# Performance work log

Measured on AMD Instinct MI355X. Metric: run time of the kernel, lower is better.

The kernel has to match this reference:

```python
import jax, jax.numpy as jnp
import numpy as np

B, N, D, DN, F, NUM_F, O, H = 8, 4096, 256, 128, 128, 1024, 8, 1024
EPS = 1e-5

def setup_inputs() -> dict:
    key = jax.random.key(0)
    ks = jax.random.split(key, 10)
    s = 0.02
    x = jax.random.normal(ks[0], (B, N, D), dtype=jnp.float32)
    ctx = jax.random.normal(ks[1], (B, DN), dtype=jnp.float32)
    idx = jax.random.randint(ks[2], (F,), 0, NUM_F, dtype=jnp.int64)
    cond_w = jax.random.normal(ks[3], (DN, 2 * D), dtype=jnp.float32) * s
    cond_b = jnp.zeros((2 * D,), dtype=jnp.float32)
    ffn_w_in = jax.random.normal(ks[4], (D, 2 * H), dtype=jnp.float32) * s
    ffn_b_in = jnp.zeros((2 * H,), dtype=jnp.float32)
    ffn_w_out = jax.random.normal(ks[5], (H, D), dtype=jnp.float32) * s
    ffn_b_out = jnp.zeros((D,), dtype=jnp.float32)
    emb = jax.random.normal(ks[6], (NUM_F, D * O), dtype=jnp.float32) * s
    return {"x": x, "ctx": ctx, "idx": idx, "cond_w": cond_w, "cond_b": cond_b,
            "ffn_w_in": ffn_w_in, "ffn_b_in": ffn_b_in,
            "ffn_w_out": ffn_w_out, "ffn_b_out": ffn_b_out, "emb": emb}

def reference(x, ctx, idx, cond_w, cond_b, ffn_w_in, ffn_b_in, ffn_w_out, ffn_b_out, emb):
    # Conditional LayerNorm: normalize over last dim, FiLM-style modulation from ctx
    mu = jnp.mean(x, axis=-1, keepdims=True)
    var = jnp.mean((x - mu) ** 2, axis=-1, keepdims=True)
    h = (x - mu) * jax.lax.rsqrt(var + EPS)                      # [B,N,D]
    ss = ctx @ cond_w + cond_b                                   # [B,2D]
    scale, shift = jnp.split(ss, 2, axis=-1)                     # [B,D] each
    h = h * (1.0 + scale[:, None, :]) + shift[:, None, :]
    # Gated FFN: in-proj -> (gelu(gate) * value) -> out-proj
    uv = h @ ffn_w_in + ffn_b_in                                 # [B,N,2H]
    u, v = jnp.split(uv, 2, axis=-1)
    y = (jax.nn.gelu(u) * v) @ ffn_w_out + ffn_b_out             # [B,N,D]
    # Embedding-generated per-feature output weights, then batched contraction
    w = emb[idx].reshape(F, D, O)                                # gather [F,D,O]
    out = jnp.einsum('bnd,fdo->bnfo', y, w)                      # [B,N,F,O]
    return out
```

## Files before the change

### kernel.cpp

```cpp
#include <hip/hip_runtime.h>
#include <cstdint>
#include <cstddef>

#define M_TOT 32768
#define D_    256
#define DN_   128
#define TWO_D 512
#define H_    1024
#define TWO_H 2048

typedef unsigned short ushort_t;
typedef __attribute__((ext_vector_type(8))) short bf16x8;
typedef __attribute__((ext_vector_type(4))) float f32x4;

__device__ __forceinline__ ushort_t f2bf(float f) {
  union { float f; uint32_t i; } v; v.f = f;
  uint32_t r = v.i + 0x7fffu + ((v.i >> 16) & 1u);
  return (ushort_t)(r >> 16);
}

__device__ __forceinline__ void async_ld16(const void* g, void* l) {
  __builtin_amdgcn_global_load_lds(
      (const __attribute__((address_space(1))) void*)g,
      (__attribute__((address_space(3))) void*)l, 16, 0, 0);
}

__global__ __launch_bounds__(256) void cond_ss_kernel(
    const float* __restrict__ ctx, const float* __restrict__ cond_w,
    const float* __restrict__ cond_b, float* __restrict__ ss) {
  int j = blockIdx.x * 256 + threadIdx.x;
  int b = j >> 9, col = j & 511;
  float acc = cond_b[col];
  for (int k = 0; k < DN_; ++k)
    acc += ctx[b * DN_ + k] * cond_w[k * TWO_D + col];
  ss[j] = acc;
}

__global__ __launch_bounds__(256) void transpose_f32_bf16_kernel(
    const float* __restrict__ in, ushort_t* __restrict__ out, int R, int C) {
  __shared__ float T[64 * 65];
  int ctiles = C >> 6;
  int bi = blockIdx.x / ctiles, bj = blockIdx.x % ctiles;
  int r0 = bi * 64, c0 = bj * 64;
  int tid = threadIdx.x;
#pragma unroll
  for (int it = 0; it < 16; ++it) {
    int idx = it * 256 + tid;
    int r = idx >> 6, c = idx & 63;
    T[r * 65 + c] = in[(size_t)(r0 + r) * C + c0 + c];
  }
  __syncthreads();
#pragma unroll
  for (int it = 0; it < 8; ++it) {
    int idx = it * 256 + tid;
    int a = idx >> 5;
    int b = (idx & 31) * 2;
    uint32_t pk = (uint32_t)f2bf(T[b * 65 + a]) |
                  ((uint32_t)f2bf(T[(b + 1) * 65 + a]) << 16);
    *(uint32_t*)&out[(size_t)(c0 + a) * R + r0 + b] = pk;
  }
}

__global__ __launch_bounds__(256) void gather_emb_kernel(
    const float* __restrict__ emb, const int* __restrict__ idx,
    ushort_t* __restrict__ W2T) {
  int f = blockIdx.x;
  bool looks64 = (idx[1] == 0) & (idx[3] == 0) & (idx[5] == 0) & (idx[7] == 0);
  int fi = looks64 ? idx[2 * f] : idx[f];
  const float* src = emb + (size_t)fi * 2048;
  int o = threadIdx.x >> 5, d0 = (threadIdx.x & 31) * 8;
  ushort_t buf[8];
#pragma unroll
  for (int k = 0; k < 8; ++k) buf[k] = f2bf(src[(d0 + k) * 8 + o]);
  *(bf16x8*)&W2T[(size_t)(f * 8 + o) * 256 + d0] = *(bf16x8*)buf;
}

__global__ __launch_bounds__(256) void ln_film_kernel(
    const float* __restrict__ x, const float* __restrict__ ss,
    ushort_t* __restrict__ h) {
  int row = blockIdx.x * 4 + (threadIdx.x >> 6);
  int lane = threadIdx.x & 63;
  int b = row >> 12;
  const float* xr = x + (size_t)row * D_;
  float4 pk = *(const float4*)(xr + lane * 4);
  float f0 = pk.x, f1 = pk.y, f2 = pk.z, f3 = pk.w;
  float s = f0 + f1 + f2 + f3;
  float q = f0 * f0 + f1 * f1 + f2 * f2 + f3 * f3;
#pragma unroll
  for (int off = 32; off > 0; off >>= 1) {
    s += __shfl_xor(s, off, 64);
    q += __shfl_xor(q, off, 64);
  }
  float mean = s * (1.0f / 256.0f);
  float var = q * (1.0f / 256.0f) - mean * mean;
  float rs = rsqrtf(var + 1e-5f);
  int d = lane * 4;
  const float* ssb = ss + b * TWO_D;
  float o0 = (f0 - mean) * rs * (1.0f + ssb[d + 0]) + ssb[256 + d + 0];
  float o1 = (f1 - mean) * rs * (1.0f + ssb[d + 1]) + ssb[256 + d + 1];
  float o2 = (f2 - mean) * rs * (1.0f + ssb[d + 2]) + ssb[256 + d + 2];
  float o3 = (f3 - mean) * rs * (1.0f + ssb[d + 3]) + ssb[256 + d + 3];
  uint2 st;
  st.x = (uint32_t)f2bf(o0) | ((uint32_t)f2bf(o1) << 16);
  st.y = (uint32_t)f2bf(o2) | ((uint32_t)f2bf(o3) << 16);
  *(uint2*)(h + (size_t)row * D_ + lane * 4) = st;
}

template <bool BIAS, bool OUT_F32>
__global__ __launch_bounds__(256, 2) void gemm_bt_kernel(
    const ushort_t* __restrict__ A, const ushort_t* __restrict__ BT,
    const float* __restrict__ bias, void* __restrict__ Cout,
    int M, int N, int K) {
  __shared__ ushort_t As[128 * 32];
  __shared__ ushort_t Bs[128 * 32];
  __shared__ float Cs[64 * 132];
  const int tid = threadIdx.x, lane = tid & 63, wave = tid >> 6;
  const int wm = wave >> 1, wn = wave & 1;
  const int m0 = blockIdx.x * 128, n0 = blockIdx.y * 128;
  const int srow = lane >> 2, sch = (lane & 3) * 8;
  f32x4 acc[4][4] = {};
  for (int k0 = 0; k0 < K; k0 += 32) {
    for (int i = wave; i < 8; i += 4) {
      async_ld16(A + (size_t)(m0 + i * 16 + srow) * K + k0 + sch, &As[i * 512]);
      async_ld16(BT + (size_t)(n0 + i * 16 + srow) * K + k0 + sch, &Bs[i * 512]);
    }
    __syncthreads();
    bf16x8 a[4], b[4];
#pragma unroll
    for (int i = 0; i < 4; ++i)
      a[i] = *(const bf16x8*)&As[(wm * 64 + i * 16 + (lane & 15)) * 32 + (lane >> 4) * 8];
#pragma unroll
    for (int j = 0; j < 4; ++j)
      b[j] = *(const bf16x8*)&Bs[(wn * 64 + j * 16 + (lane & 15)) * 32 + (lane >> 4) * 8];
#pragma unroll
    for (int i = 0; i < 4; ++i)
#pragma unroll
      for (int j = 0; j < 4; ++j)
        acc[i][j] = __builtin_amdgcn_mfma_f32_16x16x32_bf16(a[i], b[j], acc[i][j], 0, 0, 0);
    __syncthreads();
  }
#pragma unroll
  for (int p = 0; p < 2; ++p) {
    __syncthreads();
    if (wm == p) {
#pragma unroll
      for (int j = 0; j < 4; ++j) {
        int col = wn * 64 + j * 16 + (lane & 15);
        float bv = BIAS ? bias[n0 + col] : 0.0f;
#pragma unroll
        for (int i = 0; i < 4; ++i) {
          int rl = i * 16 + ((lane >> 4) << 2);
#pragma unroll
          for (int r = 0; r < 4; ++r)
            Cs[(rl + r) * 132 + col] = acc[i][j][r] + bv;
        }
      }
    }
    __syncthreads();
#pragma unroll
    for (int it = 0; it < 8; ++it) {
      int t = it * 256 + tid;
      int r = t >> 5, c = (t & 31) * 4;
      float4 v = *(const float4*)&Cs[r * 132 + c];
      size_t off = (size_t)(m0 + p * 64 + r) * N + n0 + c;
      if (OUT_F32) {
        *(float4*)((float*)Cout + off) = v;
      } else {
        ushort4 s4;
        s4.x = f2bf(v.x); s4.y = f2bf(v.y); s4.z = f2bf(v.z); s4.w = f2bf(v.w);
        *(ushort4*)((ushort_t*)Cout + off) = s4;
      }
    }
  }
}

__global__ __launch_bounds__(256, 2) void gemm_gated_kernel(
    const ushort_t* __restrict__ A,
    const ushort_t* __restrict__ WinT,
    const float* __restrict__ bin,
    ushort_t* __restrict__ G) {
  __shared__ ushort_t As[128 * 32];
  __shared__ ushort_t Bus[64 * 32];
  __shared__ ushort_t Bvs[64 * 32];
  __shared__ float Cs[64 * 68];
  const int tid = threadIdx.x, lane = tid & 63, wave = tid >> 6;
  const int wm = wave >> 1, wn = wave & 1;
  const int m0 = blockIdx.x * 128;
  const int j0 = blockIdx.y * 64;
  const int srow = lane >> 2, sch = (lane & 3) * 8;
  const int K = 256;
  f32x4 au[4][2] = {}, av[4][2] = {};
  for (int k0 = 0; k0 < K; k0 += 32) {
    for (int i = wave; i < 8; i += 4)
      async_ld16(A + (size_t)(m0 + i * 16 + srow) * K + k0 + sch, &As[i * 512]);
    {
      int i = wave;
      async_ld16(WinT + (size_t)(j0 + i * 16 + srow) * K + k0 + sch, &Bus[i * 512]);
      async_ld16(WinT + (size_t)(1024 + j0 + i * 16 + srow) * K + k0 + sch, &Bvs[i * 512]);
    }
    __syncthreads();
    bf16x8 a[4], bu[2], bv[2];
#pragma unroll
    for (int i = 0; i < 4; ++i)
      a[i] = *(const bf16x8*)&As[(wm * 64 + i * 16 + (lane & 15)) * 32 + (lane >> 4) * 8];
#pragma unroll
    for (int j = 0; j < 2; ++j) {
      bu[j] = *(const bf16x8*)&Bus[(wn * 32 + j * 16 + (lane & 15)) * 32 + (lane >> 4) * 8];
      bv[j] = *(const bf16x8*)&Bvs[(wn * 32 + j * 16 + (lane & 15)) * 32 + (lane >> 4) * 8];
    }
#pragma unroll
    for (int i = 0; i < 4; ++i)
#pragma unroll
      for (int j = 0; j < 2; ++j) {
        au[i][j] = __builtin_amdgcn_mfma_f32_16x16x32_bf16(a[i], bu[j], au[i][j], 0, 0, 0);
        av[i][j] = __builtin_amdgcn_mfma_f32_16x16x32_bf16(a[i], bv[j], av[i][j], 0, 0, 0);
      }
    __syncthreads();
  }
#pragma unroll
  for (int p = 0; p < 2; ++p) {
    __syncthreads();
    if (wm == p) {
#pragma unroll
      for (int j = 0; j < 2; ++j) {
        int col = wn * 32 + j * 16 + (lane & 15);
        float bub = bin[j0 + col];
        float bvb = bin[1024 + j0 + col];
#pragma unroll
        for (int i = 0; i < 4; ++i) {
          int rl = i * 16 + ((lane >> 4) << 2);
#pragma unroll
          for (int r = 0; r < 4; ++r) {
            float u = au[i][j][r] + bub;
            float v = av[i][j][r] + bvb;
            float t = 0.7978845608028654f * (u + 0.044715f * u * u * u);
            float e = __expf(2.0f * t);
            float th = 1.0f - 2.0f / (e + 1.0f);
            float gl = 0.5f * u * (1.0f + th);
            Cs[(rl + r) * 68 + col] = gl * v;
          }
        }
      }
    }
    __syncthreads();
#pragma unroll
    for (int it = 0; it < 4; ++it) {
      int t = it * 256 + tid;
      int r = t >> 4, c = (t & 15) * 4;
      float4 v = *(const float4*)&Cs[r * 68 + c];
      ushort4 s4;
      s4.x = f2bf(v.x); s4.y = f2bf(v.y); s4.z = f2bf(v.z); s4.w = f2bf(v.w);
      *(ushort4*)&G[(size_t)(m0 + p * 64 + r) * 1024 + j0 + c] = s4;
    }
  }
}

extern "C" void kernel_launch(void* const* d_in, const int* in_sizes, int n_in,
                              void* d_out, int out_size, void* d_ws, size_t ws_size,
                              hipStream_t stream) {
  const float* x      = (const float*)d_in[0];
  const float* ctx    = (const float*)d_in[1];
  const int*   idx    = (const int*)d_in[2];
  const float* cond_w = (const float*)d_in[3];
  const float* cond_b = (const float*)d_in[4];
  const float* w_in   = (const float*)d_in[5];
  const float* b_in   = (const float*)d_in[6];
  const float* w_out  = (const float*)d_in[7];
  const float* b_out  = (const float*)d_in[8];
  const float* emb    = (const float*)d_in[9];

  char* w = (char*)d_ws;
  float* ss = (float*)w;           w += (size_t)8 * TWO_D * 4;
  ushort_t* h = (ushort_t*)w;      w += (size_t)M_TOT * D_ * 2;
  ushort_t* y = (ushort_t*)w;      w += (size_t)M_TOT * D_ * 2;
  ushort_t* WinT = (ushort_t*)w;   w += (size_t)TWO_H * D_ * 2;
  ushort_t* WoutT = (ushort_t*)w;  w += (size_t)D_ * H_ * 2;
  ushort_t* W2T = (ushort_t*)w;    w += (size_t)H_ * D_ * 2;
  ushort_t* g = (ushort_t*)d_out;

  cond_ss_kernel<<<16, 256, 0, stream>>>(ctx, cond_w, cond_b, ss);
  transpose_f32_bf16_kernel<<<(D_ / 64) * (TWO_H / 64), 256, 0, stream>>>(w_in, WinT, D_, TWO_H);
  transpose_f32_bf16_kernel<<<(H_ / 64) * (D_ / 64), 256, 0, stream>>>(w_out, WoutT, H_, D_);
  gather_emb_kernel<<<128, 256, 0, stream>>>(emb, idx, W2T);
  ln_film_kernel<<<M_TOT / 4, 256, 0, stream>>>(x, ss, h);
  gemm_gated_kernel<<<dim3(256, 16), 256, 0, stream>>>(h, WinT, b_in, g);
  gemm_bt_kernel<true, false><<<dim3(256, 2), 256, 0, stream>>>(g, WoutT, b_out, y, M_TOT, 256, 1024);
  gemm_bt_kernel<false, true><<<dim3(256, 8), 256, 0, stream>>>(y, W2T, nullptr, d_out, M_TOT, 1024, 256);
}
```

Before: 319.3 us.

## Fuse gated FFN in-proj and out-proj into one kernel keeping intermediate on-chip

Replaces the separate gated in-projection GEMM and the out-projection GEMM with one fused kernel. Each 64-row block keeps its LN output in LDS and loops over H in chunks of 64, computing the gelu-gated intermediate into LDS and accumulating the 256-wide output in registers. This removes the write and re-read of the 32768x1024 bf16 intermediate through global memory. The final GEMM now loads K in steps of 64 to halve barrier count. In exchange the fused kernel uses smaller M tiles, many barriers per block, large LDS footprint (lower occupancy), and only 512 blocks, which may hurt MFMA utilization.

```diff
diff --git a/kernel.cpp b/kernel.cpp
--- a/kernel.cpp
+++ b/kernel.cpp
@@ -106,37 +106,140 @@
   *(uint2*)(h + (size_t)row * D_ + lane * 4) = st;
 }
 
-template <bool BIAS, bool OUT_F32>
-__global__ __launch_bounds__(256, 2) void gemm_bt_kernel(
+__global__ __launch_bounds__(256, 2) void ffn_fused_kernel(
+    const ushort_t* __restrict__ h,
+    const ushort_t* __restrict__ WinT,
+    const float* __restrict__ bin,
+    const ushort_t* __restrict__ WoutT,
+    const float* __restrict__ bout,
+    ushort_t* __restrict__ y) {
+  __shared__ ushort_t Ah[64 * 256];
+  __shared__ ushort_t Sh[64 * 264];
+  __shared__ ushort_t Gs[64 * 72];
+  const int tid = threadIdx.x, lane = tid & 63, wave = tid >> 6;
+  const int r = lane >> 2, q = lane & 3;
+  const int l15 = lane & 15, l4 = lane >> 4;
+  const int m0 = blockIdx.x * 64;
+  const int fragoff = l15 * 32 + l4 * 8;
+
+  for (int t = wave; t < 32; t += 4) {
+    int rt = t & 3, kc = t >> 2;
+    async_ld16(h + (size_t)(m0 + rt * 16 + r) * 256 + kc * 32 + q * 8, &Ah[t * 512]);
+  }
+
+  f32x4 yac[16] = {};
+
+  for (int j = 0; j < 16; ++j) {
+    f32x4 uac[4] = {}, vac[4] = {};
+#pragma unroll
+    for (int s = 0; s < 2; ++s) {
+      __syncthreads();
+      for (int t = wave; t < 16; t += 4) {
+        int rt = t & 3, kc = t >> 2;
+        size_t grow = (size_t)(j * 64 + rt * 16 + r);
+        async_ld16(WinT + grow * 256 + s * 128 + kc * 32 + q * 8, &Sh[t * 512]);
+        async_ld16(WinT + (grow + 1024) * 256 + s * 128 + kc * 32 + q * 8, &Sh[(16 + t) * 512]);
+      }
+      __syncthreads();
+#pragma unroll
+      for (int ks = 0; ks < 4; ++ks) {
+        bf16x8 af = *(const bf16x8*)&Ah[((s * 4 + ks) * 4 + wave) * 512 + fragoff];
+#pragma unroll
+        for (int jt = 0; jt < 4; ++jt) {
+          bf16x8 bu = *(const bf16x8*)&Sh[(ks * 4 + jt) * 512 + fragoff];
+          bf16x8 bv = *(const bf16x8*)&Sh[(16 + ks * 4 + jt) * 512 + fragoff];
+          uac[jt] = __builtin_amdgcn_mfma_f32_16x16x32_bf16(af, bu, uac[jt], 0, 0, 0);
+          vac[jt] = __builtin_amdgcn_mfma_f32_16x16x32_bf16(af, bv, vac[jt], 0, 0, 0);
+        }
+      }
+    }
+#pragma unroll
+    for (int jt = 0; jt < 4; ++jt) {
+      int col = jt * 16 + l15;
+      float bub = bin[j * 64 + col];
+      float bvb = bin[1024 + j * 64 + col];
+#pragma unroll
+      for (int rr = 0; rr < 4; ++rr) {
+        float u = uac[jt][rr] + bub;
+        float v = vac[jt][rr] + bvb;
+        float t = 0.7978845608028654f * (u + 0.044715f * u * u * u);
+        float e = __expf(2.0f * t);
+        float th = 1.0f - 2.0f / (e + 1.0f);
+        float gl = 0.5f * u * (1.0f + th);
+        Gs[(wave * 16 + l4 * 4 + rr) * 72 + col] = f2bf(gl * v);
+      }
+    }
+    __syncthreads();
+    for (int t = wave; t < 32; t += 4) {
+      int nt = t & 15, s2 = t >> 4;
+      async_ld16(WoutT + (size_t)(nt * 16 + r) * 1024 + j * 64 + s2 * 32 + q * 8, &Sh[t * 512]);
+    }
+    __syncthreads();
+#pragma unroll
+    for (int s2 = 0; s2 < 2; ++s2) {
+      bf16x8 gf = *(const bf16x8*)&Gs[(wave * 16 + l15) * 72 + s2 * 32 + l4 * 8];
+#pragma unroll
+      for (int nt = 0; nt < 16; ++nt) {
+        bf16x8 bw = *(const bf16x8*)&Sh[(s2 * 16 + nt) * 512 + fragoff];
+        yac[nt] = __builtin_amdgcn_mfma_f32_16x16x32_bf16(gf, bw, yac[nt], 0, 0, 0);
+      }
+    }
+  }
+  __syncthreads();
+#pragma unroll
+  for (int nt = 0; nt < 16; ++nt) {
+    int col = nt * 16 + l15;
+    float bb = bout[col];
+#pragma unroll
+    for (int rr = 0; rr < 4; ++rr)
+      Sh[(wave * 16 + l4 * 4 + rr) * 264 + col] = f2bf(yac[nt][rr] + bb);
+  }
+  __syncthreads();
+#pragma unroll
+  for (int it = 0; it < 8; ++it) {
+    int id = it * 256 + tid;
+    int rr = id >> 5, cc = id & 31;
+    bf16x8 vv = *(const bf16x8*)&Sh[rr * 264 + cc * 8];
+    *(bf16x8*)&y[(size_t)(m0 + rr) * 256 + cc * 8] = vv;
+  }
+}
+
+__global__ __launch_bounds__(256, 2) void gemm_out_kernel(
     const ushort_t* __restrict__ A, const ushort_t* __restrict__ BT,
-    const float* __restrict__ bias, void* __restrict__ Cout,
-    int M, int N, int K) {
-  __shared__ ushort_t As[128 * 32];
-  __shared__ ushort_t Bs[128 * 32];
+    float* __restrict__ C) {
+  __shared__ ushort_t As[128 * 64];
+  __shared__ ushort_t Bs[128 * 64];
   __shared__ float Cs[64 * 132];
   const int tid = threadIdx.x, lane = tid & 63, wave = tid >> 6;
   const int wm = wave >> 1, wn = wave & 1;
   const int m0 = blockIdx.x * 128, n0 = blockIdx.y * 128;
-  const int srow = lane >> 2, sch = (lane & 3) * 8;
+  const int r = lane >> 2, q = lane & 3;
+  const int l15 = lane & 15, l4 = lane >> 4;
+  const int fragoff = l15 * 32 + l4 * 8;
+  const int N = 1024, K = 256;
   f32x4 acc[4][4] = {};
-  for (int k0 = 0; k0 < K; k0 += 32) {
-    for (int i = wave; i < 8; i += 4) {
-      async_ld16(A + (size_t)(m0 + i * 16 + srow) * K + k0 + sch, &As[i * 512]);
-      async_ld16(BT + (size_t)(n0 + i * 16 + srow) * K + k0 + sch, &Bs[i * 512]);
-    }
-    __syncthreads();
-    bf16x8 a[4], b[4];
-#pragma unroll
-    for (int i = 0; i < 4; ++i)
-      a[i] = *(const bf16x8*)&As[(wm * 64 + i * 16 + (lane & 15)) * 32 + (lane >> 4) * 8];
-#pragma unroll
-    for (int j = 0; j < 4; ++j)
-      b[j] = *(const bf16x8*)&Bs[(wn * 64 + j * 16 + (lane & 15)) * 32 + (lane >> 4) * 8];
-#pragma unroll
-    for (int i = 0; i < 4; ++i)
-#pragma unroll
-      for (int j = 0; j < 4; ++j)
-        acc[i][j] = __builtin_amdgcn_mfma_f32_16x16x32_bf16(a[i], b[j], acc[i][j], 0, 0, 0);
+  for (int k0 = 0; k0 < K; k0 += 64) {
+    for (int t = wave; t < 16; t += 4) {
+      int rt = t >> 1, ks = t & 1;
+      async_ld16(A + (size_t)(m0 + rt * 16 + r) * K + k0 + ks * 32 + q * 8, &As[t * 512]);
+      async_ld16(BT + (size_t)(n0 + rt * 16 + r) * K + k0 + ks * 32 + q * 8, &Bs[t * 512]);
+    }
+    __syncthreads();
+#pragma unroll
+    for (int ks = 0; ks < 2; ++ks) {
+      bf16x8 a[4], b[4];
+#pragma unroll
+      for (int i = 0; i < 4; ++i)
+        a[i] = *(const bf16x8*)&As[((wm * 4 + i) * 2 + ks) * 512 + fragoff];
+#pragma unroll
+      for (int jt = 0; jt < 4; ++jt)
+        b[jt] = *(const bf16x8*)&Bs[((wn * 4 + jt) * 2 + ks) * 512 + fragoff];
+#pragma unroll
+      for (int i = 0; i < 4; ++i)
+#pragma unroll
+        for (int jt = 0; jt < 4; ++jt)
+          acc[i][jt] = __builtin_amdgcn_mfma_f32_16x16x32_bf16(a[i], b[jt], acc[i][jt], 0, 0, 0);
+    }
     __syncthreads();
   }
 #pragma unroll
@@ -144,15 +247,14 @@
     __syncthreads();
     if (wm == p) {
 #pragma unroll
-      for (int j = 0; j < 4; ++j) {
-        int col = wn * 64 + j * 16 + (lane & 15);
-        float bv = BIAS ? bias[n0 + col] : 0.0f;
+      for (int jt = 0; jt < 4; ++jt) {
+        int col = wn * 64 + jt * 16 + l15;
 #pragma unroll
         for (int i = 0; i < 4; ++i) {
-          int rl = i * 16 + ((lane >> 4) << 2);
-#pragma unroll
-          for (int r = 0; r < 4; ++r)
-            Cs[(rl + r) * 132 + col] = acc[i][j][r] + bv;
+          int rl = i * 16 + (l4 << 2);
+#pragma unroll
+          for (int rr = 0; rr < 4; ++rr)
+            Cs[(rl + rr) * 132 + col] = acc[i][jt][rr];
         }
       }
     }
@@ -160,97 +262,9 @@
 #pragma unroll
     for (int it = 0; it < 8; ++it) {
       int t = it * 256 + tid;
-      int r = t >> 5, c = (t & 31) * 4;
-      float4 v = *(const float4*)&Cs[r * 132 + c];
-      size_t off = (size_t)(m0 + p * 64 + r) * N + n0 + c;
-      if (OUT_F32) {
-        *(float4*)((float*)Cout + off) = v;
-      } else {
-        ushort4 s4;
-        s4.x = f2bf(v.x); s4.y = f2bf(v.y); s4.z = f2bf(v.z); s4.w = f2bf(v.w);
-        *(ushort4*)((ushort_t*)Cout + off) = s4;
-      }
-    }
-  }
-}
-
-__global__ __launch_bounds__(256, 2) void gemm_gated_kernel(
-    const ushort_t* __restrict__ A,
-    const ushort_t* __restrict__ WinT,
-    const float* __restrict__ bin,
-    ushort_t* __restrict__ G) {
-  __shared__ ushort_t As[128 * 32];
-  __shared__ ushort_t Bus[64 * 32];
-  __shared__ ushort_t Bvs[64 * 32];
-  __shared__ float Cs[64 * 68];
-  const int tid = threadIdx.x, lane = tid & 63, wave = tid >> 6;
-  const int wm = wave >> 1, wn = wave & 1;
-  const int m0 = blockIdx.x * 128;
-  const int j0 = blockIdx.y * 64;
-  const int srow = lane >> 2, sch = (lane & 3) * 8;
-  const int K = 256;
-  f32x4 au[4][2] = {}, av[4][2] = {};
-  for (int k0 = 0; k0 < K; k0 += 32) {
-    for (int i = wave; i < 8; i += 4)
-      async_ld16(A + (size_t)(m0 + i * 16 + srow) * K + k0 + sch, &As[i * 512]);
-    {
-      int i = wave;
-      async_ld16(WinT + (size_t)(j0 + i * 16 + srow) * K + k0 + sch, &Bus[i * 512]);
-      async_ld16(WinT + (size_t)(1024 + j0 + i * 16 + srow) * K + k0 + sch, &Bvs[i * 512]);
-    }
-    __syncthreads();
-    bf16x8 a[4], bu[2], bv[2];
-#pragma unroll
-    for (int i = 0; i < 4; ++i)
-      a[i] = *(const bf16x8*)&As[(wm * 64 + i * 16 + (lane & 15)) * 32 + (lane >> 4) * 8];
-#pragma unroll
-    for (int j = 0; j < 2; ++j) {
-      bu[j] = *(const bf16x8*)&Bus[(wn * 32 + j * 16 + (lane & 15)) * 32 + (lane >> 4) * 8];
-      bv[j] = *(const bf16x8*)&Bvs[(wn * 32 + j * 16 + (lane & 15)) * 32 + (lane >> 4) * 8];
-    }
-#pragma unroll
-    for (int i = 0; i < 4; ++i)
-#pragma unroll
-      for (int j = 0; j < 2; ++j) {
-        au[i][j] = __builtin_amdgcn_mfma_f32_16x16x32_bf16(a[i], bu[j], au[i][j], 0, 0, 0);
-        av[i][j] = __builtin_amdgcn_mfma_f32_16x16x32_bf16(a[i], bv[j], av[i][j], 0, 0, 0);
-      }
-    __syncthreads();
-  }
-#pragma unroll
-  for (int p = 0; p < 2; ++p) {
-    __syncthreads();
-    if (wm == p) {
-#pragma unroll
-      for (int j = 0; j < 2; ++j) {
-        int col = wn * 32 + j * 16 + (lane & 15);
-        float bub = bin[j0 + col];
-        float bvb = bin[1024 + j0 + col];
-#pragma unroll
-        for (int i = 0; i < 4; ++i) {
-          int rl = i * 16 + ((lane >> 4) << 2);
-#pragma unroll
-          for (int r = 0; r < 4; ++r) {
-            float u = au[i][j][r] + bub;
-            float v = av[i][j][r] + bvb;
-            float t = 0.7978845608028654f * (u + 0.044715f * u * u * u);
-            float e = __expf(2.0f * t);
-            float th = 1.0f - 2.0f / (e + 1.0f);
-            float gl = 0.5f * u * (1.0f + th);
-            Cs[(rl + r) * 68 + col] = gl * v;
-          }
-        }
-      }
-    }
-    __syncthreads();
-#pragma unroll
-    for (int it = 0; it < 4; ++it) {
-      int t = it * 256 + tid;
-      int r = t >> 4, c = (t & 15) * 4;
-      float4 v = *(const float4*)&Cs[r * 68 + c];
-      ushort4 s4;
-      s4.x = f2bf(v.x); s4.y = f2bf(v.y); s4.z = f2bf(v.z); s4.w = f2bf(v.w);
-      *(ushort4*)&G[(size_t)(m0 + p * 64 + r) * 1024 + j0 + c] = s4;
+      int rr = t >> 5, c = (t & 31) * 4;
+      float4 v = *(const float4*)&Cs[rr * 132 + c];
+      *(float4*)&C[(size_t)(m0 + p * 64 + rr) * N + n0 + c] = v;
     }
   }
 }
@@ -276,14 +290,12 @@
   ushort_t* WinT = (ushort_t*)w;   w += (size_t)TWO_H * D_ * 2;
   ushort_t* WoutT = (ushort_t*)w;  w += (size_t)D_ * H_ * 2;
   ushort_t* W2T = (ushort_t*)w;    w += (size_t)H_ * D_ * 2;
-  ushort_t* g = (ushort_t*)d_out;
 
   cond_ss_kernel<<<16, 256, 0, stream>>>(ctx, cond_w, cond_b, ss);
   transpose_f32_bf16_kernel<<<(D_ / 64) * (TWO_H / 64), 256, 0, stream>>>(w_in, WinT, D_, TWO_H);
   transpose_f32_bf16_kernel<<<(H_ / 64) * (D_ / 64), 256, 0, stream>>>(w_out, WoutT, H_, D_);
   gather_emb_kernel<<<128, 256, 0, stream>>>(emb, idx, W2T);
   ln_film_kernel<<<M_TOT / 4, 256, 0, stream>>>(x, ss, h);
-  gemm_gated_kernel<<<dim3(256, 16), 256, 0, stream>>>(h, WinT, b_in, g);
-  gemm_bt_kernel<true, false><<<dim3(256, 2), 256, 0, stream>>>(g, WoutT, b_out, y, M_TOT, 256, 1024);
-  gemm_bt_kernel<false, true><<<dim3(256, 8), 256, 0, stream>>>(y, W2T, nullptr, d_out, M_TOT, 1024, 256);
-}
+  ffn_fused_kernel<<<M_TOT / 64, 256, 0, stream>>>(h, WinT, b_in, WoutT, b_out, y);
+  gemm_out_kernel<<<dim3(M_TOT / 128, H_ / 128), 256, 0, stream>>>(y, W2T, (float*)d_out);
+}
```

New measurement: 307.2 us. 3.8% less time.
